# Optimization experiments

Measured on AMD Instinct MI355X. Metric: run time of the kernel, lower is better.

The kernel has to match this reference:

```python
import jax, jax.numpy as jnp
import numpy as np

B, S, D_IN = 2, 2048, 1024
H, DH = 16, 64          # num_heads, hidden_size (per-head dim)
D_MODEL = H * DH        # 1024
D_OUT = DH * 8          # 512


def setup_inputs() -> dict:
    key = jax.random.key(0)
    ks = jax.random.split(key, 9)
    s_in = 1.0 / np.sqrt(D_IN)
    s_md = 1.0 / np.sqrt(D_MODEL)
    return {
        "x": jax.random.normal(ks[0], (B, S, D_IN), dtype=jnp.float32),
        "Wq": jax.random.uniform(ks[1], (D_IN, D_MODEL), jnp.float32, -s_in, s_in),
        "bq": jax.random.uniform(ks[2], (D_MODEL,), jnp.float32, -s_in, s_in),
        "Wk": jax.random.uniform(ks[3], (D_IN, D_MODEL), jnp.float32, -s_in, s_in),
        "bk": jax.random.uniform(ks[4], (D_MODEL,), jnp.float32, -s_in, s_in),
        "Wv": jax.random.uniform(ks[5], (D_IN, D_MODEL), jnp.float32, -s_in, s_in),
        "bv": jax.random.uniform(ks[6], (D_MODEL,), jnp.float32, -s_in, s_in),
        "Wo": jax.random.uniform(ks[7], (D_MODEL, D_OUT), jnp.float32, -s_md, s_md),
        "bo": jax.random.uniform(ks[8], (D_OUT,), jnp.float32, -s_md, s_md),
    }


def reference(x, Wq, bq, Wk, bk, Wv, bv, Wo, bo):
    b, s, _ = x.shape
    # QKV projections -> [B, H, S, DH]
    def proj(W, bias):
        y = jnp.einsum("bsd,de->bse", x, W) + bias
        return y.reshape(b, s, H, DH).transpose(0, 2, 1, 3)
    Q, K, V = proj(Wq, bq), proj(Wk, bk), proj(Wv, bv)
    scores = jnp.einsum("bhqd,bhkd->bhqk", Q, K) / jnp.sqrt(jnp.float32(DH))
    weights = jax.nn.softmax(scores, axis=-1)
    attn = jnp.einsum("bhqk,bhkd->bhqd", weights, V)  # [B, H, S, DH]
    attn = attn.transpose(0, 2, 1, 3).reshape(b, s, H * DH)
    return jnp.einsum("bsd,de->bse", attn, Wo) + bo
```

## Files before the change

### kernel.cpp

```cpp
#include <hip/hip_runtime.h>

typedef __attribute__((ext_vector_type(8))) __bf16 bf16x8;
typedef __attribute__((ext_vector_type(4))) __bf16 bf16x4;
typedef __attribute__((ext_vector_type(4))) float f32x4;

#define MFMA16x16x32(A, B, C) __builtin_amdgcn_mfma_f32_16x16x32_bf16(A, B, C, 0, 0, 0)

__device__ __forceinline__ unsigned short f2bf(float f) {
    unsigned int u = __float_as_uint(f);
    u += 0x7fffu + ((u >> 16) & 1u);
    return (unsigned short)(u >> 16);
}

__device__ __forceinline__ unsigned cvtpk_bf16(float lo, float hi) {
    unsigned r;
    asm("v_cvt_pk_bf16_f32 %0, %1, %2" : "=v"(r) : "v"(lo), "v"(hi));
    return r;
}

__device__ __forceinline__ float exp2_hw(float x) {
    float r;
    asm("v_exp_f32 %0, %1" : "=v"(r) : "v"(x));
    return r;
}

__device__ __forceinline__ void gload16(const void* src, void* lds) {
    __builtin_amdgcn_global_load_lds(
        (const __attribute__((address_space(1))) unsigned int*)src,
        (__attribute__((address_space(3))) unsigned int*)lds,
        16, 0, 0);
}

__global__ __launch_bounds__(256) void prep_kernel(
    const float* __restrict__ x, unsigned short* __restrict__ xb,
    const float* __restrict__ Wq, const float* __restrict__ Wk,
    const float* __restrict__ Wv, const float* __restrict__ Wo,
    unsigned short* __restrict__ Wqt, unsigned short* __restrict__ Wkt,
    unsigned short* __restrict__ Wvt, unsigned short* __restrict__ Wot)
{
    __shared__ float tile[32][33];
    const int blk = blockIdx.x;
    const int tid = threadIdx.x;

    if (blk < 4096) {
        const int i = (blk * 256 + tid) * 4;
        const float4 v = *(const float4*)(x + i);
        ushort4 o;
        o.x = f2bf(v.x); o.y = f2bf(v.y); o.z = f2bf(v.z); o.w = f2bf(v.w);
        *(ushort4*)(xb + i) = o;
        return;
    }

    const int blk2 = blk - 4096;
    const int kx = blk2 & 31;
    int y = blk2 >> 5;
    const float* W; unsigned short* Wt; int N;
    if (y < 32)      { W = Wq; Wt = Wqt; N = 1024; }
    else if (y < 64) { W = Wk; Wt = Wkt; N = 1024; y -= 32; }
    else if (y < 96) { W = Wv; Wt = Wvt; N = 1024; y -= 64; }
    else             { W = Wo; Wt = Wot; N = 512;  y -= 96; }
    const int k0 = kx * 32;
    const int n0 = y * 32;
    const int tx = tid & 31, ty = tid >> 5;
#pragma unroll
    for (int i = 0; i < 4; ++i)
        tile[ty + 8 * i][tx] = W[(size_t)(k0 + ty + 8 * i) * N + n0 + tx];
    __syncthreads();
#pragma unroll
    for (int i = 0; i < 4; ++i)
        Wt[(size_t)(n0 + ty + 8 * i) * 1024 + k0 + tx] = f2bf(tile[tx][ty + 8 * i]);
}

__global__ __launch_bounds__(256, 3) void gemm_qkv_kernel(
    const unsigned short* __restrict__ xb,
    const unsigned short* __restrict__ Wqt,
    const unsigned short* __restrict__ Wkt,
    const unsigned short* __restrict__ Wvt,
    const float* __restrict__ bq, const float* __restrict__ bk, const float* __restrict__ bv,
    unsigned short* __restrict__ Qb, unsigned short* __restrict__ Kb, unsigned short* __restrict__ Vt)
{
    __shared__ unsigned short sA[2][128 * 32];
    __shared__ unsigned short sB[2][128 * 32];

    const int tid  = threadIdx.x;
    const int lane = tid & 63;
    const int w    = tid >> 6;
    const int wm   = w >> 1, wn = w & 1;
    const int li   = lane & 15, gg = lane >> 4;

    const int L  = blockIdx.y * 24 + blockIdx.x;
    const int v  = (L & 7) * 96 + (L >> 3);
    const int vx = v >> 5;
    const int vy = v & 31;
    const int m0    = vy * 128;
    const int which = vx >> 3;
    const int nloc0 = (vx & 7) * 128;

    const unsigned short* Wt = (which == 0) ? Wqt : ((which == 1) ? Wkt : Wvt);
    const float* bias        = (which == 0) ? bq  : ((which == 1) ? bk  : bv);
    const float osc          = (which == 0) ? 0.18033688011112042f : 1.0f;

    const int srow = lane >> 2;
    const int schk = lane & 3;

    f32x4 acc[4][4];
#pragma unroll
    for (int i = 0; i < 4; ++i)
#pragma unroll
        for (int j = 0; j < 4; ++j)
            acc[i][j] = (f32x4){0.f, 0.f, 0.f, 0.f};

    int aoff[4], boff[4];
#pragma unroll
    for (int f = 0; f < 4; ++f) {
        const int ra = wm * 64 + f * 16 + li;
        aoff[f] = ra * 32 + ((gg ^ ((ra >> 1) & 3)) * 8);
        const int rb = wn * 64 + f * 16 + li;
        boff[f] = rb * 32 + ((gg ^ ((rb >> 1) & 3)) * 8);
    }

#pragma unroll
    for (int j = 0; j < 2; ++j) {
        const int rl = (w * 2 + j) * 16 + srow;
        const int c  = schk ^ ((rl >> 1) & 3);
        gload16(xb + (size_t)(m0 + rl) * 1024 + c * 8,   sA[0] + (w * 2 + j) * 512);
        gload16(Wt + (size_t)(nloc0 + rl) * 1024 + c * 8, sB[0] + (w * 2 + j) * 512);
    }
    __syncthreads();

    for (int kt = 0; kt < 32; ++kt) {
        const int cur = kt & 1;
        if (kt < 31) {
            const int k1 = (kt + 1) * 32;
#pragma unroll
            for (int j = 0; j < 2; ++j) {
                const int rl = (w * 2 + j) * 16 + srow;
                const int c  = schk ^ ((rl >> 1) & 3);
                gload16(xb + (size_t)(m0 + rl) * 1024 + k1 + c * 8,   sA[cur ^ 1] + (w * 2 + j) * 512);
                gload16(Wt + (size_t)(nloc0 + rl) * 1024 + k1 + c * 8, sB[cur ^ 1] + (w * 2 + j) * 512);
            }
        }
        bf16x8 av[4], bw[4];
#pragma unroll
        for (int f = 0; f < 4; ++f) av[f] = *(const bf16x8*)(sA[cur] + aoff[f]);
#pragma unroll
        for (int f = 0; f < 4; ++f) bw[f] = *(const bf16x8*)(sB[cur] + boff[f]);
#pragma unroll
        for (int mf = 0; mf < 4; ++mf)
#pragma unroll
            for (int nf = 0; nf < 4; ++nf)
                acc[mf][nf] = MFMA16x16x32(av[mf], bw[nf], acc[mf][nf]);
        __syncthreads();
    }

    if (which == 2) {
#pragma unroll
        for (int nf = 0; nf < 4; ++nf) {
            const int nl = nloc0 + wn * 64 + nf * 16 + li;
            const float bi = bias[nl];
            const int h = nl >> 6, d = nl & 63;
#pragma unroll
            for (int mf = 0; mf < 4; ++mf) {
                const int m = m0 + wm * 64 + mf * 16 + gg * 4;
                const int b = m >> 11, s0 = m & 2047;
                ushort4 o;
                o.x = f2bf(acc[mf][nf][0] + bi);
                o.y = f2bf(acc[mf][nf][1] + bi);
                o.z = f2bf(acc[mf][nf][2] + bi);
                o.w = f2bf(acc[mf][nf][3] + bi);
                *(ushort4*)(Vt + (((size_t)(b * 16 + h)) * 64 + d) * 2048 + s0) = o;
            }
        }
    } else {
        unsigned short* dst = (which == 0) ? Qb : Kb;
#pragma unroll
        for (int nf = 0; nf < 4; ++nf) {
            const int nl = nloc0 + wn * 64 + nf * 16 + li;
            const float bi = bias[nl];
            const int h = nl >> 6, d = nl & 63;
#pragma unroll
            for (int mf = 0; mf < 4; ++mf) {
#pragma unroll
                for (int r = 0; r < 4; ++r) {
                    const int m = m0 + wm * 64 + mf * 16 + gg * 4 + r;
                    const int b = m >> 11, s = m & 2047;
                    dst[(((size_t)(b * 16 + h)) * 2048 + s) * 64 + d] = f2bf((acc[mf][nf][r] + bi) * osc);
                }
            }
        }
    }
}

__global__ __launch_bounds__(512, 4) void attn_kernel(
    const unsigned short* __restrict__ Qb,
    const unsigned short* __restrict__ Kb,
    const unsigned short* __restrict__ Vt,
    unsigned short* __restrict__ Ob)
{
    __shared__ unsigned short sK[2][2][64 * 64];
    __shared__ unsigned short sV[2][2][64 * 64];

    const int tid  = threadIdx.x;
    const int lane = tid & 63;
    const int w    = tid >> 6;
    const int li   = lane & 15, gg = lane >> 4;

    const int L  = blockIdx.y * 16 + blockIdx.x;
    const int v  = (L & 7) * 64 + (L >> 3);
    const int bh = v >> 4;
    const int q0 = (v & 15) * 128 + w * 16;

    const int slot = w * 64 + lane;
    const int srow = slot >> 3;
    const int schk = (slot & 7) ^ (srow & 7);

    const unsigned short* Kbase = Kb + ((size_t)bh * 2048 + srow) * 64 + schk * 8;
    const unsigned short* Vbase = Vt + ((size_t)bh * 64 + srow) * 2048 + schk * 8;

    bf16x8 qf[2];
#pragma unroll
    for (int kk = 0; kk < 2; ++kk) {
        const int q = q0 + li;
        const int d = kk * 32 + gg * 8;
        qf[kk] = *(const bf16x8*)(Qb + ((size_t)bh * 2048 + q) * 64 + d);
    }

    f32x4 acc[4];
#pragma unroll
    for (int df = 0; df < 4; ++df) acc[df] = (f32x4){0.f, 0.f, 0.f, 0.f};
    float l_s = 0.f;

    gload16(Kbase,                     sK[0][0] + slot * 8);
    gload16(Kbase + 64 * 64,           sK[0][1] + slot * 8);
    gload16(Vbase,                     sV[0][0] + slot * 8);
    gload16(Vbase + 64,                sV[0][1] + slot * 8);
    __syncthreads();

    for (int tt = 0; tt < 16; ++tt) {
        const int cur = tt & 1;
        if (tt < 15) {
            const size_t ko = (size_t)(tt + 1) * 8192;
            const size_t vo = (size_t)(tt + 1) * 128;
            gload16(Kbase + ko,            sK[cur ^ 1][0] + slot * 8);
            gload16(Kbase + ko + 4096,     sK[cur ^ 1][1] + slot * 8);
            gload16(Vbase + vo,            sV[cur ^ 1][0] + slot * 8);
            gload16(Vbase + vo + 64,       sV[cur ^ 1][1] + slot * 8);
        }

#pragma unroll
        for (int sub = 0; sub < 2; ++sub) {
            const unsigned short* sKh = sK[cur][sub];
            const unsigned short* sVh = sV[cur][sub];

            bf16x8 kf[4][2];
#pragma unroll
            for (int nf = 0; nf < 4; ++nf)
#pragma unroll
                for (int kk = 0; kk < 2; ++kk) {
                    const int n = nf * 16 + li;
                    const int ch = kk * 4 + gg;
                    kf[nf][kk] = *(const bf16x8*)(sKh + n * 64 + ((ch ^ (n & 7)) * 8));
                }
            f32x4 st[4];
            __builtin_amdgcn_s_setprio(1);
#pragma unroll
            for (int nf = 0; nf < 4; ++nf) {
                st[nf] = (f32x4){0.f, 0.f, 0.f, 0.f};
                st[nf] = MFMA16x16x32(kf[nf][0], qf[0], st[nf]);
                st[nf] = MFMA16x16x32(kf[nf][1], qf[1], st[nf]);
            }
            __builtin_amdgcn_s_setprio(0);

            float rs = 0.f;
            unsigned pk[4][2];
#pragma unroll
            for (int nf = 0; nf < 4; ++nf) {
#pragma unroll
                for (int r = 0; r < 4; ++r) {
                    const float p = exp2_hw(st[nf][r]);
                    st[nf][r] = p;
                    rs += p;
                }
                pk[nf][0] = cvtpk_bf16(st[nf][0], st[nf][1]);
                pk[nf][1] = cvtpk_bf16(st[nf][2], st[nf][3]);
            }
            l_s += rs;

            bf16x8 pf[2];
#pragma unroll
            for (int kk = 0; kk < 2; ++kk) {
                unsigned A = pk[2 * kk][0], C = pk[2 * kk + 1][0];
                unsigned B = pk[2 * kk][1], D = pk[2 * kk + 1][1];
                asm("v_permlane32_swap_b32 %0, %1" : "+v"(A), "+v"(C));
                asm("v_permlane16_swap_b32 %0, %1" : "+v"(A), "+v"(C));
                asm("v_permlane32_swap_b32 %0, %1" : "+v"(B), "+v"(D));
                asm("v_permlane16_swap_b32 %0, %1" : "+v"(B), "+v"(D));
                uint4 u;
                u.x = A; u.y = B; u.z = C; u.w = D;
                pf[kk] = *reinterpret_cast<bf16x8*>(&u);
            }

            bf16x8 vf[4][2];
#pragma unroll
            for (int df = 0; df < 4; ++df)
#pragma unroll
                for (int kk = 0; kk < 2; ++kk) {
                    const int n = df * 16 + li;
                    const int ch = kk * 4 + gg;
                    vf[df][kk] = *(const bf16x8*)(sVh + n * 64 + ((ch ^ (n & 7)) * 8));
                }
            __builtin_amdgcn_s_setprio(1);
#pragma unroll
            for (int df = 0; df < 4; ++df) {
                acc[df] = MFMA16x16x32(pf[0], vf[df][0], acc[df]);
                acc[df] = MFMA16x16x32(pf[1], vf[df][1], acc[df]);
            }
            __builtin_amdgcn_s_setprio(0);
        }
        __syncthreads();
    }

    float lf = l_s;
    lf += __shfl_xor(lf, 16, 64);
    lf += __shfl_xor(lf, 32, 64);

    const int b = bh >> 4, h = bh & 15;
#pragma unroll
    for (int r = 0; r < 4; ++r) {
        const float lbc = __shfl(lf, gg * 4 + r, 64);
        const float rl = 1.0f / lbc;
        const int q = q0 + gg * 4 + r;
#pragma unroll
        for (int df = 0; df < 4; ++df) {
            const int d = df * 16 + li;
            Ob[(((size_t)b * 2048 + q) * 16 + h) * 64 + d] = f2bf(acc[df][r] * rl);
        }
    }
}

__global__ __launch_bounds__(256, 2) void gemm_out_kernel(
    const unsigned short* __restrict__ attn,
    const unsigned short* __restrict__ Wot,
    const float* __restrict__ bo,
    float* __restrict__ out)
{
    __shared__ unsigned short sA[2][64 * 32];
    __shared__ unsigned short sB[2][128 * 32];

    const int tid  = threadIdx.x;
    const int lane = tid & 63;
    const int w    = tid >> 6;
    const int wm   = w >> 1, wn = w & 1;
    const int li   = lane & 15, gg = lane >> 4;
    const int m0   = blockIdx.y * 64;
    const int n0   = blockIdx.x * 128;

    const int arow = tid >> 2;
    const int acol = tid & 3;

    f32x4 acc[2][4];
#pragma unroll
    for (int i = 0; i < 2; ++i)
#pragma unroll
        for (int j = 0; j < 4; ++j)
            acc[i][j] = (f32x4){0.f, 0.f, 0.f, 0.f};

    int aoff[2], boff[4];
#pragma unroll
    for (int f = 0; f < 2; ++f) {
        const int ra = wm * 32 + f * 16 + li;
        aoff[f] = ra * 32 + ((gg ^ ((ra >> 1) & 3)) * 8);
    }
#pragma unroll
    for (int f = 0; f < 4; ++f) {
        const int rb = wn * 64 + f * 16 + li;
        boff[f] = rb * 32 + ((gg ^ ((rb >> 1) & 3)) * 8);
    }

    {
        const int ca = acol ^ ((arow >> 1) & 3);
        gload16(attn + (size_t)(m0 + arow) * 1024 + ca * 8, sA[0] + tid * 8);
#pragma unroll
        for (int jj = 0; jj < 2; ++jj) {
            const int rb = jj * 64 + arow;
            const int cb = acol ^ ((rb >> 1) & 3);
            gload16(Wot + (size_t)(n0 + rb) * 1024 + cb * 8, sB[0] + (jj * 256 + tid) * 8);
        }
    }
    __syncthreads();

    for (int kt = 0; kt < 32; ++kt) {
        const int cur = kt & 1;
        if (kt < 31) {
            const int k1 = (kt + 1) * 32;
            const int ca = acol ^ ((arow >> 1) & 3);
            gload16(attn + (size_t)(m0 + arow) * 1024 + k1 + ca * 8, sA[cur ^ 1] + tid * 8);
#pragma unroll
            for (int jj = 0; jj < 2; ++jj) {
                const int rb = jj * 64 + arow;
                const int cb = acol ^ ((rb >> 1) & 3);
                gload16(Wot + (size_t)(n0 + rb) * 1024 + k1 + cb * 8, sB[cur ^ 1] + (jj * 256 + tid) * 8);
            }
        }
        bf16x8 av[2], bw[4];
#pragma unroll
        for (int f = 0; f < 2; ++f) av[f] = *(const bf16x8*)(sA[cur] + aoff[f]);
#pragma unroll
        for (int f = 0; f < 4; ++f) bw[f] = *(const bf16x8*)(sB[cur] + boff[f]);
#pragma unroll
        for (int mf = 0; mf < 2; ++mf)
#pragma unroll
            for (int nf = 0; nf < 4; ++nf)
                acc[mf][nf] = MFMA16x16x32(av[mf], bw[nf], acc[mf][nf]);
        __syncthreads();
    }

#pragma unroll
    for (int nf = 0; nf < 4; ++nf) {
        const int n = n0 + wn * 64 + nf * 16 + li;
        const float bi = bo[n];
#pragma unroll
        for (int mf = 0; mf < 2; ++mf) {
#pragma unroll
            for (int r = 0; r < 4; ++r) {
                const int m = m0 + wm * 32 + mf * 16 + gg * 4 + r;
                out[(size_t)m * 512 + n] = acc[mf][nf][r] + bi;
            }
        }
    }
}

extern "C" void kernel_launch(void* const* d_in, const int* in_sizes, int n_in,
                              void* d_out, int out_size, void* d_ws, size_t ws_size,
                              hipStream_t stream) {
    const float* x  = (const float*)d_in[0];
    const float* Wq = (const float*)d_in[1];
    const float* bq = (const float*)d_in[2];
    const float* Wk = (const float*)d_in[3];
    const float* bk = (const float*)d_in[4];
    const float* Wv = (const float*)d_in[5];
    const float* bv = (const float*)d_in[6];
    const float* Wo = (const float*)d_in[7];
    const float* bo = (const float*)d_in[8];
    float* out = (float*)d_out;

    unsigned short* ws  = (unsigned short*)d_ws;
    unsigned short* xb  = ws;
    unsigned short* Wqt = xb  + 4194304;
    unsigned short* Wkt = Wqt + 1048576;
    unsigned short* Wvt = Wkt + 1048576;
    unsigned short* Wot = Wvt + 1048576;
    unsigned short* Qb  = Wot + 524288;
    unsigned short* Kb  = Qb  + 4194304;
    unsigned short* Vt  = Kb  + 4194304;
    unsigned short* attnb = Vt + 4194304;

    prep_kernel<<<dim3(7680), dim3(256), 0, stream>>>(x, xb, Wq, Wk, Wv, Wo,
                                                      Wqt, Wkt, Wvt, Wot);
    gemm_qkv_kernel<<<dim3(24, 32), dim3(256), 0, stream>>>(xb, Wqt, Wkt, Wvt,
                                                            bq, bk, bv, Qb, Kb, Vt);
    attn_kernel<<<dim3(16, 32), dim3(512), 0, stream>>>(Qb, Kb, Vt, attnb);
    gemm_out_kernel<<<dim3(4, 64), dim3(256), 0, stream>>>(attnb, Wot, bo, out);
}
```

Before: 108.0 us.

## Process two query fragments per warp in attention to reuse K/V tiles

Each attention warp now computes 32 query rows (two 16-row fragments) against every staged K/V tile, doubling the query tile per block to 256 and halving the grid to 256 blocks. This halves global K/V loads and LDS fragment reads per query, amortizing them over more MFMA work. In exchange, register pressure rises, launch bounds drop to 2 waves per SIMD, and the smaller grid gives roughly one block per CU, reducing latency hiding.

```diff
diff --git a/kernel.cpp b/kernel.cpp
--- a/kernel.cpp
+++ b/kernel.cpp
@@ -191,7 +191,7 @@
     }
 }
 
-__global__ __launch_bounds__(512, 4) void attn_kernel(
+__global__ __launch_bounds__(512, 2) void attn_kernel(
     const unsigned short* __restrict__ Qb,
     const unsigned short* __restrict__ Kb,
     const unsigned short* __restrict__ Vt,
@@ -205,35 +205,41 @@
     const int w    = tid >> 6;
     const int li   = lane & 15, gg = lane >> 4;
 
-    const int L  = blockIdx.y * 16 + blockIdx.x;
-    const int v  = (L & 7) * 64 + (L >> 3);
-    const int bh = v >> 4;
-    const int q0 = (v & 15) * 128 + w * 16;
-
-    const int slot = w * 64 + lane;
+    const int L  = blockIdx.x;
+    const int v  = (L & 7) * 32 + (L >> 3);
+    const int bh = v >> 3;
+    const int q0 = (v & 7) * 256 + w * 32;
+
+    const int slot = tid;
     const int srow = slot >> 3;
     const int schk = (slot & 7) ^ (srow & 7);
 
     const unsigned short* Kbase = Kb + ((size_t)bh * 2048 + srow) * 64 + schk * 8;
     const unsigned short* Vbase = Vt + ((size_t)bh * 64 + srow) * 2048 + schk * 8;
 
-    bf16x8 qf[2];
-#pragma unroll
-    for (int kk = 0; kk < 2; ++kk) {
-        const int q = q0 + li;
-        const int d = kk * 32 + gg * 8;
-        qf[kk] = *(const bf16x8*)(Qb + ((size_t)bh * 2048 + q) * 64 + d);
-    }
-
-    f32x4 acc[4];
-#pragma unroll
-    for (int df = 0; df < 4; ++df) acc[df] = (f32x4){0.f, 0.f, 0.f, 0.f};
-    float l_s = 0.f;
-
-    gload16(Kbase,                     sK[0][0] + slot * 8);
-    gload16(Kbase + 64 * 64,           sK[0][1] + slot * 8);
-    gload16(Vbase,                     sV[0][0] + slot * 8);
-    gload16(Vbase + 64,                sV[0][1] + slot * 8);
+    bf16x8 qf[2][2];
+#pragma unroll
+    for (int mq = 0; mq < 2; ++mq)
+#pragma unroll
+        for (int kk = 0; kk < 2; ++kk) {
+            const int q = q0 + mq * 16 + li;
+            const int d = kk * 32 + gg * 8;
+            qf[mq][kk] = *(const bf16x8*)(Qb + ((size_t)bh * 2048 + q) * 64 + d);
+        }
+
+    f32x4 acc[2][4];
+    float l_s[2];
+#pragma unroll
+    for (int mq = 0; mq < 2; ++mq) {
+#pragma unroll
+        for (int df = 0; df < 4; ++df) acc[mq][df] = (f32x4){0.f, 0.f, 0.f, 0.f};
+        l_s[mq] = 0.f;
+    }
+
+    gload16(Kbase,          sK[0][0] + slot * 8);
+    gload16(Kbase + 4096,   sK[0][1] + slot * 8);
+    gload16(Vbase,          sV[0][0] + slot * 8);
+    gload16(Vbase + 64,     sV[0][1] + slot * 8);
     __syncthreads();
 
     for (int tt = 0; tt < 16; ++tt) {
@@ -241,10 +247,10 @@
         if (tt < 15) {
             const size_t ko = (size_t)(tt + 1) * 8192;
             const size_t vo = (size_t)(tt + 1) * 128;
-            gload16(Kbase + ko,            sK[cur ^ 1][0] + slot * 8);
-            gload16(Kbase + ko + 4096,     sK[cur ^ 1][1] + slot * 8);
-            gload16(Vbase + vo,            sV[cur ^ 1][0] + slot * 8);
-            gload16(Vbase + vo + 64,       sV[cur ^ 1][1] + slot * 8);
+            gload16(Kbase + ko,        sK[cur ^ 1][0] + slot * 8);
+            gload16(Kbase + ko + 4096, sK[cur ^ 1][1] + slot * 8);
+            gload16(Vbase + vo,        sV[cur ^ 1][0] + slot * 8);
+            gload16(Vbase + vo + 64,   sV[cur ^ 1][1] + slot * 8);
         }
 
 #pragma unroll
@@ -261,43 +267,47 @@
                     const int ch = kk * 4 + gg;
                     kf[nf][kk] = *(const bf16x8*)(sKh + n * 64 + ((ch ^ (n & 7)) * 8));
                 }
-            f32x4 st[4];
-            __builtin_amdgcn_s_setprio(1);
-#pragma unroll
-            for (int nf = 0; nf < 4; ++nf) {
-                st[nf] = (f32x4){0.f, 0.f, 0.f, 0.f};
-                st[nf] = MFMA16x16x32(kf[nf][0], qf[0], st[nf]);
-                st[nf] = MFMA16x16x32(kf[nf][1], qf[1], st[nf]);
-            }
-            __builtin_amdgcn_s_setprio(0);
-
-            float rs = 0.f;
-            unsigned pk[4][2];
-#pragma unroll
-            for (int nf = 0; nf < 4; ++nf) {
-#pragma unroll
-                for (int r = 0; r < 4; ++r) {
-                    const float p = exp2_hw(st[nf][r]);
-                    st[nf][r] = p;
-                    rs += p;
-                }
-                pk[nf][0] = cvtpk_bf16(st[nf][0], st[nf][1]);
-                pk[nf][1] = cvtpk_bf16(st[nf][2], st[nf][3]);
-            }
-            l_s += rs;
-
-            bf16x8 pf[2];
-#pragma unroll
-            for (int kk = 0; kk < 2; ++kk) {
-                unsigned A = pk[2 * kk][0], C = pk[2 * kk + 1][0];
-                unsigned B = pk[2 * kk][1], D = pk[2 * kk + 1][1];
-                asm("v_permlane32_swap_b32 %0, %1" : "+v"(A), "+v"(C));
-                asm("v_permlane16_swap_b32 %0, %1" : "+v"(A), "+v"(C));
-                asm("v_permlane32_swap_b32 %0, %1" : "+v"(B), "+v"(D));
-                asm("v_permlane16_swap_b32 %0, %1" : "+v"(B), "+v"(D));
-                uint4 u;
-                u.x = A; u.y = B; u.z = C; u.w = D;
-                pf[kk] = *reinterpret_cast<bf16x8*>(&u);
+
+            bf16x8 pf[2][2];
+#pragma unroll
+            for (int mq = 0; mq < 2; ++mq) {
+                f32x4 st[4];
+                __builtin_amdgcn_s_setprio(1);
+#pragma unroll
+                for (int nf = 0; nf < 4; ++nf) {
+                    st[nf] = (f32x4){0.f, 0.f, 0.f, 0.f};
+                    st[nf] = MFMA16x16x32(kf[nf][0], qf[mq][0], st[nf]);
+                    st[nf] = MFMA16x16x32(kf[nf][1], qf[mq][1], st[nf]);
+                }
+                __builtin_amdgcn_s_setprio(0);
+
+                float rs = 0.f;
+                unsigned pk[4][2];
+#pragma unroll
+                for (int nf = 0; nf < 4; ++nf) {
+#pragma unroll
+                    for (int r = 0; r < 4; ++r) {
+                        const float p = exp2_hw(st[nf][r]);
+                        st[nf][r] = p;
+                        rs += p;
+                    }
+                    pk[nf][0] = cvtpk_bf16(st[nf][0], st[nf][1]);
+                    pk[nf][1] = cvtpk_bf16(st[nf][2], st[nf][3]);
+                }
+                l_s[mq] += rs;
+
+#pragma unroll
+                for (int kk = 0; kk < 2; ++kk) {
+                    unsigned A = pk[2 * kk][0], C = pk[2 * kk + 1][0];
+                    unsigned B = pk[2 * kk][1], D = pk[2 * kk + 1][1];
+                    asm("v_permlane32_swap_b32 %0, %1" : "+v"(A), "+v"(C));
+                    asm("v_permlane16_swap_b32 %0, %1" : "+v"(A), "+v"(C));
+                    asm("v_permlane32_swap_b32 %0, %1" : "+v"(B), "+v"(D));
+                    asm("v_permlane16_swap_b32 %0, %1" : "+v"(B), "+v"(D));
+                    uint4 u;
+                    u.x = A; u.y = B; u.z = C; u.w = D;
+                    pf[mq][kk] = *reinterpret_cast<bf16x8*>(&u);
+                }
             }
 
             bf16x8 vf[4][2];
@@ -311,29 +321,33 @@
                 }
             __builtin_amdgcn_s_setprio(1);
 #pragma unroll
+            for (int mq = 0; mq < 2; ++mq)
+#pragma unroll
+                for (int df = 0; df < 4; ++df) {
+                    acc[mq][df] = MFMA16x16x32(pf[mq][0], vf[df][0], acc[mq][df]);
+                    acc[mq][df] = MFMA16x16x32(pf[mq][1], vf[df][1], acc[mq][df]);
+                }
+            __builtin_amdgcn_s_setprio(0);
+        }
+        __syncthreads();
+    }
+
+    const int b = bh >> 4, h = bh & 15;
+#pragma unroll
+    for (int mq = 0; mq < 2; ++mq) {
+        float lf = l_s[mq];
+        lf += __shfl_xor(lf, 16, 64);
+        lf += __shfl_xor(lf, 32, 64);
+#pragma unroll
+        for (int r = 0; r < 4; ++r) {
+            const float lbc = __shfl(lf, gg * 4 + r, 64);
+            const float rl = 1.0f / lbc;
+            const int q = q0 + mq * 16 + gg * 4 + r;
+#pragma unroll
             for (int df = 0; df < 4; ++df) {
-                acc[df] = MFMA16x16x32(pf[0], vf[df][0], acc[df]);
-                acc[df] = MFMA16x16x32(pf[1], vf[df][1], acc[df]);
-            }
-            __builtin_amdgcn_s_setprio(0);
-        }
-        __syncthreads();
-    }
-
-    float lf = l_s;
-    lf += __shfl_xor(lf, 16, 64);
-    lf += __shfl_xor(lf, 32, 64);
-
-    const int b = bh >> 4, h = bh & 15;
-#pragma unroll
-    for (int r = 0; r < 4; ++r) {
-        const float lbc = __shfl(lf, gg * 4 + r, 64);
-        const float rl = 1.0f / lbc;
-        const int q = q0 + gg * 4 + r;
-#pragma unroll
-        for (int df = 0; df < 4; ++df) {
-            const int d = df * 16 + li;
-            Ob[(((size_t)b * 2048 + q) * 16 + h) * 64 + d] = f2bf(acc[df][r] * rl);
+                const int d = df * 16 + li;
+                Ob[(((size_t)b * 2048 + q) * 16 + h) * 64 + d] = f2bf(acc[mq][df][r] * rl);
+            }
         }
     }
 }
@@ -459,6 +473,6 @@
                                                       Wqt, Wkt, Wvt, Wot);
     gemm_qkv_kernel<<<dim3(24, 32), dim3(256), 0, stream>>>(xb, Wqt, Wkt, Wvt,
                                                             bq, bk, bv, Qb, Kb, Vt);
-    attn_kernel<<<dim3(16, 32), dim3(512), 0, stream>>>(Qb, Kb, Vt, attnb);
+    attn_kernel<<<dim3(256), dim3(512), 0, stream>>>(Qb, Kb, Vt, attnb);
     gemm_out_kernel<<<dim3(4, 64), dim3(256), 0, stream>>>(attnb, Wot, bo, out);
 }
```

After: 108.3 us. About the same (+0.3%).
